# Optimization experiments

Hardware: AMD Instinct MI355X
Metric: run time of the kernel (lower is better)

## Reference

```python
import jax, jax.numpy as jnp
import numpy as np

N_NODES = 10000
N_EDGES = 160000
IN_DIM = 512
HID = 128
HEADS = 8
EMB = 256
NEG_SLOPE = 0.2  # PyG GATConv default


def setup_inputs() -> dict:
    key = jax.random.key(0)
    ks = jax.random.split(key, 12)
    x = jax.random.normal(ks[0], (N_NODES, IN_DIM), dtype=jnp.float32)
    edge_index = jax.random.randint(ks[1], (2, N_EDGES), 0, N_NODES, dtype=jnp.int64)
    s1 = 1.0 / np.sqrt(IN_DIM)
    s2 = 1.0 / np.sqrt(HEADS * HID)
    W1 = jax.random.normal(ks[2], (IN_DIM, HEADS * HID), dtype=jnp.float32) * s1
    a_src1 = jax.random.normal(ks[3], (HEADS, HID), dtype=jnp.float32) * s2
    a_dst1 = jax.random.normal(ks[4], (HEADS, HID), dtype=jnp.float32) * s2
    b1 = jnp.zeros((HEADS * HID,), dtype=jnp.float32)
    W2 = jax.random.normal(ks[5], (HEADS * HID, EMB), dtype=jnp.float32) * s2
    a_src2 = jax.random.normal(ks[6], (1, EMB), dtype=jnp.float32) * (1.0 / np.sqrt(EMB))
    a_dst2 = jax.random.normal(ks[7], (1, EMB), dtype=jnp.float32) * (1.0 / np.sqrt(EMB))
    b2 = jnp.zeros((EMB,), dtype=jnp.float32)
    return {"x": x, "edge_index": edge_index, "W1": W1, "a_src1": a_src1,
            "a_dst1": a_dst1, "b1": b1, "W2": W2, "a_src2": a_src2,
            "a_dst2": a_dst2, "b2": b2}


def gat_layer(h_in, src, dst, W, a_src, a_dst, b, concat, num_nodes):
    """PyG-style GATConv (eval mode, self-loops already in src/dst)."""
    H, C = a_src.shape
    h = (h_in @ W).reshape(num_nodes, H, C)            # [N, H, C]
    alpha_src = jnp.einsum('nhc,hc->nh', h, a_src)      # [N, H]
    alpha_dst = jnp.einsum('nhc,hc->nh', h, a_dst)      # [N, H]
    e = jax.nn.leaky_relu(alpha_src[src] + alpha_dst[dst], NEG_SLOPE)  # [E, H]
    # segment softmax over incoming edges of each destination node
    m = jax.ops.segment_max(e, dst, num_segments=num_nodes)            # [N, H]
    ex = jnp.exp(e - m[dst])
    denom = jax.ops.segment_sum(ex, dst, num_segments=num_nodes)       # [N, H]
    alpha = ex / denom[dst]                                            # [E, H]
    out = jax.ops.segment_sum(h[src] * alpha[:, :, None], dst,
                              num_segments=num_nodes)                  # [N, H, C]
    out = out.reshape(num_nodes, H * C) if concat else out.mean(axis=1)
    return out + b


def reference(x, edge_index, W1, a_src1, a_dst1, b1, W2, a_src2, a_dst2, b2):
    N = x.shape[0]
    loops = jnp.arange(N, dtype=edge_index.dtype)
    src = jnp.concatenate([edge_index[0], loops])
    dst = jnp.concatenate([edge_index[1], loops])
    h = gat_layer(x, src, dst, W1, a_src1, a_dst1, b1, concat=True, num_nodes=N)
    h = jax.nn.elu(h)  # dropout inactive in eval mode
    out = gat_layer(h, src, dst, W2, a_src2, a_dst2, b2, concat=False, num_nodes=N)
    return out
```

## Files before the change

kernel.cpp:

```cpp
#include <hip/hip_runtime.h>
#include <hip/hip_bf16.h>

typedef __attribute__((ext_vector_type(8))) short short8;
typedef __attribute__((ext_vector_type(4))) float floatx4;
typedef __attribute__((ext_vector_type(4))) unsigned short ushort4v;
typedef __attribute__((ext_vector_type(8))) unsigned short ushort8v;
typedef __attribute__((ext_vector_type(2))) unsigned int uint2v;
typedef __attribute__((ext_vector_type(4))) unsigned int uint4v;

#define NN 10000
#define E0 160000
#define ETOT (E0 + NN)
#define IN_DIM 512
#define HID1 1024
#define EMB 256
#define MPAD 10112
#define NX (NN * IN_DIM)
#define NW1 (IN_DIM * HID1)
#define NW2 (HID1 * EMB)
#define DETB 625

__device__ __forceinline__ float bf2f(unsigned short u) {
    unsigned v = ((unsigned)u) << 16;
    float f;
    __builtin_memcpy(&f, &v, 4);
    return f;
}
__device__ __forceinline__ float bflo(unsigned v) {
    unsigned x = v << 16;
    float f; __builtin_memcpy(&f, &x, 4);
    return f;
}
__device__ __forceinline__ float bfhi(unsigned v) {
    unsigned x = v & 0xffff0000u;
    float f; __builtin_memcpy(&f, &x, 4);
    return f;
}
__device__ __forceinline__ unsigned short f2bf(float f) {
    unsigned u;
    __builtin_memcpy(&u, &f, 4);
    unsigned lsb = (u >> 16) & 1;
    u += 0x7fff + lsb;
    return (unsigned short)(u >> 16);
}
__device__ __forceinline__ unsigned packbf(float lo, float hi) {
    return (unsigned)f2bf(lo) | ((unsigned)f2bf(hi) << 16);
}
__device__ __forceinline__ float loadf(const void* p, size_t i, int isf32) {
    if (isf32) return ((const float*)p)[i];
    return bf2f(((const unsigned short*)p)[i]);
}
__device__ __forceinline__ float lrelu(float e) { return e > 0.f ? e : 0.2f * e; }

__global__ void zero_kernel(int* p, int n) {
    int i = blockIdx.x * 256 + threadIdx.x;
    if (i < n) p[i] = 0;
}

__global__ __launch_bounds__(256) void probe_kernel(const int* ei32, const unsigned* xw,
                                                    int* eflag, int* isf32) {
    int t = threadIdx.x;
    if (blockIdx.x < DETB) {
        int i = blockIdx.x * 256 + t;
        int v = 0;
        int idx = 2 * i + 1;
        if (idx < 2 * E0) v = ei32[idx];
        unsigned long long any = __ballot(v != 0);
        if (any && (t & 63) == 0) atomicOr(eflag, 1);
    } else {
        __shared__ int cnt[256];
        int c = 0;
        #pragma unroll
        for (int j = 0; j < 16; ++j) {
            unsigned w = xw[t * 16 + j];
            int ex = (w >> 7) & 0xFF;
            if (ex >= 110 && ex <= 135) c++;
        }
        cnt[t] = c;
        __syncthreads();
        for (int off = 128; off > 0; off >>= 1) {
            if (t < off) cnt[t] += cnt[t + off];
            __syncthreads();
        }
        if (t == 0) *isf32 = (cnt[0] < 2048) ? 1 : 0;
    }
}

__device__ __forceinline__ int load_edge(const void* ei, long long idx, int m32) {
    if (m32) return ((const int*)ei)[idx];
    return (int)(((const long long*)ei)[idx]);
}

__global__ void count_kernel(const void* ei, const int* flag, int* counts) {
    int e = blockIdx.x * 256 + threadIdx.x;
    if (e < E0) {
        int m32 = (*flag != 0);
        int d = load_edge(ei, (long long)E0 + e, m32);
        if (d >= 0 && d < NN) atomicAdd(&counts[d], 1);
    }
}

__global__ __launch_bounds__(1024) void scan_kernel(const int* counts, int* offsets, int* cursor) {
    __shared__ int wsum[16];
    int t = threadIdx.x;
    int lane = t & 63, wv = t >> 6;
    int base = t * 10;
    int local[10];
    int s = 0;
    #pragma unroll
    for (int j = 0; j < 10; ++j) {
        int idx = base + j;
        int v = (idx < NN) ? (counts[idx] + 1) : 0;
        local[j] = v; s += v;
    }
    int v = s;
    #pragma unroll
    for (int d = 1; d < 64; d <<= 1) {
        int o = __shfl_up(v, d, 64);
        if (lane >= d) v += o;
    }
    if (lane == 63) wsum[wv] = v;
    __syncthreads();
    if (t < 16) {
        int w = wsum[t];
        #pragma unroll
        for (int d = 1; d < 16; d <<= 1) {
            int o = __shfl_up(w, d, 16);
            if (t >= d) w += o;
        }
        wsum[t] = w;
    }
    __syncthreads();
    int woff = (wv == 0) ? 0 : wsum[wv - 1];
    int run = woff + v - s;
    #pragma unroll
    for (int j = 0; j < 10; ++j) {
        int idx = base + j;
        if (idx < NN) { offsets[idx] = run; cursor[idx] = run; run += local[j]; }
    }
    if (t == 1023) offsets[NN] = wsum[15];
}

__global__ void scatter_kernel(const void* ei, const int* flag, int* cursor, int* csr_src) {
    int e = blockIdx.x * 256 + threadIdx.x;
    if (e >= ETOT) return;
    int m32 = (*flag != 0);
    int s, d;
    if (e < E0) { s = load_edge(ei, e, m32); d = load_edge(ei, (long long)E0 + e, m32); }
    else { s = d = e - E0; }
    if (s < 0) s = 0; if (s >= NN) s = NN - 1;
    if (d < 0) d = 0; if (d >= NN) d = NN - 1;
    int pos = atomicAdd(&cursor[d], 1);
    if (pos >= 0 && pos < ETOT) csr_src[pos] = s;
}

__global__ void convall_kernel(const void* x, const void* W1, const void* W2,
                               unsigned short* xb, unsigned short* W1t, unsigned short* W2t,
                               const int* isf32)
{
    int i = blockIdx.x * 256 + threadIdx.x;
    int f = *isf32;
    if (i < NX) { xb[i] = f2bf(loadf(x, i, f)); return; }
    i -= NX;
    if (i < NW1) {
        int r = i / HID1, c = i % HID1;
        W1t[(size_t)c * IN_DIM + r] = f2bf(loadf(W1, i, f));
        return;
    }
    i -= NW1;
    if (i < NW2) {
        int r = i / EMB, c = i % EMB;
        W2t[(size_t)c * HID1 + r] = f2bf(loadf(W2, i, f));
    }
}

template<bool OUTBF16>
__global__ __launch_bounds__(256) void gemm_tile(
    const unsigned short* __restrict__ A,
    const unsigned short* __restrict__ Bt,
    void* __restrict__ Cv,
    int N, int K)
{
    __shared__ unsigned short As[128 * 32];
    __shared__ unsigned short Bs[128 * 32];
    int t = threadIdx.x;
    int wave = t >> 6;
    int lane = t & 63;
    int quad = lane >> 4;
    int l16  = lane & 15;
    int mq = wave & 1, nq = wave >> 1;
    size_t mblk = (size_t)blockIdx.x * 128;
    size_t nblk = (size_t)blockIdx.y * 128;

    floatx4 acc[4][4];
    #pragma unroll
    for (int i = 0; i < 4; ++i)
        #pragma unroll
        for (int j = 0; j < 4; ++j)
            acc[i][j] = (floatx4){0.f, 0.f, 0.f, 0.f};

    const unsigned short* Abase = A + mblk * K;
    const unsigned short* Bbase = Bt + nblk * K;

    for (int kk = 0; kk < K; kk += 32) {
        __syncthreads();
        #pragma unroll
        for (int j = 0; j < 2; ++j) {
            int chunk = (wave << 7) + (j << 6) + lane;
            int r  = chunk >> 2;
            int cs = (chunk & 3) ^ (r & 3);
            const unsigned short* ga = Abase + (size_t)r * K + kk + cs * 8;
            const unsigned short* gb = Bbase + (size_t)r * K + kk + cs * 8;
            __builtin_amdgcn_global_load_lds(
                (const __attribute__((address_space(1))) void*)ga,
                (__attribute__((address_space(3))) void*)(As + (size_t)((wave << 7) + (j << 6)) * 8),
                16, 0, 0);
            __builtin_amdgcn_global_load_lds(
                (const __attribute__((address_space(1))) void*)gb,
                (__attribute__((address_space(3))) void*)(Bs + (size_t)((wave << 7) + (j << 6)) * 8),
                16, 0, 0);
        }
        __syncthreads();

        short8 af[4], bf[4];
        #pragma unroll
        for (int i = 0; i < 4; ++i) {
            int ar = mq * 64 + i * 16 + l16;
            int br = nq * 64 + i * 16 + l16;
            af[i] = *(const short8*)(const void*)(As + ar * 32 + (quad ^ (ar & 3)) * 8);
            bf[i] = *(const short8*)(const void*)(Bs + br * 32 + (quad ^ (br & 3)) * 8);
        }
        #pragma unroll
        for (int i = 0; i < 4; ++i)
            #pragma unroll
            for (int j = 0; j < 4; ++j)
                acc[i][j] = __builtin_amdgcn_mfma_f32_16x16x32_bf16(af[i], bf[j], acc[i][j], 0, 0, 0);
    }

    size_t crow0 = mblk + mq * 64 + quad * 4;
    size_t ccol0 = nblk + nq * 64 + l16;
    #pragma unroll
    for (int i = 0; i < 4; ++i) {
        #pragma unroll
        for (int r = 0; r < 4; ++r) {
            size_t row = crow0 + i * 16 + r;
            size_t b = row * N + ccol0;
            #pragma unroll
            for (int j = 0; j < 4; ++j) {
                if (OUTBF16) ((unsigned short*)Cv)[b + j * 16] = f2bf(acc[i][j][r]);
                else         ((float*)Cv)[b + j * 16] = acc[i][j][r];
            }
        }
    }
}

__global__ __launch_bounds__(256) void alpha1_kernel(
    const unsigned short* __restrict__ h1,
    const void* __restrict__ a_src, const void* __restrict__ a_dst,
    const int* __restrict__ isf32,
    float* __restrict__ as1, float* __restrict__ ad1)
{
    int n = blockIdx.x, t = threadIdx.x;
    int f = *isf32;
    ushort4v hv = *(const ushort4v*)(const void*)(h1 + (size_t)n * HID1 + t * 4);
    float ps = 0.f, pd = 0.f;
    #pragma unroll
    for (int i = 0; i < 4; ++i) {
        float h = bf2f(hv[i]);
        ps += h * loadf(a_src, t * 4 + i, f);
        pd += h * loadf(a_dst, t * 4 + i, f);
    }
    #pragma unroll
    for (int off = 1; off < 32; off <<= 1) {
        ps += __shfl_xor(ps, off, 64);
        pd += __shfl_xor(pd, off, 64);
    }
    if ((t & 31) == 0) {
        int h = t >> 5;
        as1[n * 8 + h] = ps;
        ad1[n * 8 + h] = pd;
    }
}

__global__ __launch_bounds__(256) void agg1_kernel(
    const unsigned short* __restrict__ h1, const int* __restrict__ offsets,
    const int* __restrict__ csr_src, const float* __restrict__ as1,
    const float* __restrict__ ad1, const void* __restrict__ b1,
    const int* __restrict__ isf32,
    unsigned short* __restrict__ hmid)
{
    int head = blockIdx.x & 7;
    int ng   = blockIdx.x >> 3;
    int n    = ng * 4 + (threadIdx.x >> 6);
    if (n >= NN) return;
    int lane = threadIdx.x & 63;
    int q    = lane >> 4;
    int sl   = lane & 15;
    int f = *isf32;
    int beg = offsets[n], end = offsets[n + 1];
    if (beg < 0) beg = 0; if (end > ETOT) end = ETOT;
    float ad = ad1[n * 8 + head];
    const unsigned* rb = (const unsigned*)h1 + head * 64 + sl * 4;
    const float* asb = as1 + head;

    float den = 0.f;
    float acc[8];
    #pragma unroll
    for (int j = 0; j < 8; ++j) acc[j] = 0.f;

    int i = beg + q;
    for (; i + 12 < end; i += 16) {
        int s0 = csr_src[i];      s0 &= 0x7fffffff; if (s0 >= NN) s0 = 0;
        int s1 = csr_src[i + 4];  s1 &= 0x7fffffff; if (s1 >= NN) s1 = 0;
        int s2 = csr_src[i + 8];  s2 &= 0x7fffffff; if (s2 >= NN) s2 = 0;
        int s3 = csr_src[i + 12]; s3 &= 0x7fffffff; if (s3 >= NN) s3 = 0;
        uint4v v0 = *(const uint4v*)(const void*)(rb + (size_t)s0 * 512);
        uint4v v1 = *(const uint4v*)(const void*)(rb + (size_t)s1 * 512);
        uint4v v2 = *(const uint4v*)(const void*)(rb + (size_t)s2 * 512);
        uint4v v3 = *(const uint4v*)(const void*)(rb + (size_t)s3 * 512);
        float w0 = __expf(lrelu(asb[s0 * 8] + ad));
        float w1 = __expf(lrelu(asb[s1 * 8] + ad));
        float w2 = __expf(lrelu(asb[s2 * 8] + ad));
        float w3 = __expf(lrelu(asb[s3 * 8] + ad));
        den += (w0 + w1) + (w2 + w3);
        #pragma unroll
        for (int k = 0; k < 4; ++k) {
            acc[2 * k]     += (bflo(v0[k]) * w0 + bflo(v1[k]) * w1) + (bflo(v2[k]) * w2 + bflo(v3[k]) * w3);
            acc[2 * k + 1] += (bfhi(v0[k]) * w0 + bfhi(v1[k]) * w1) + (bfhi(v2[k]) * w2 + bfhi(v3[k]) * w3);
        }
    }
    for (; i + 4 < end; i += 8) {
        int s0 = csr_src[i];     s0 &= 0x7fffffff; if (s0 >= NN) s0 = 0;
        int s1 = csr_src[i + 4]; s1 &= 0x7fffffff; if (s1 >= NN) s1 = 0;
        uint4v v0 = *(const uint4v*)(const void*)(rb + (size_t)s0 * 512);
        uint4v v1 = *(const uint4v*)(const void*)(rb + (size_t)s1 * 512);
        float w0 = __expf(lrelu(asb[s0 * 8] + ad));
        float w1 = __expf(lrelu(asb[s1 * 8] + ad));
        den += w0 + w1;
        #pragma unroll
        for (int k = 0; k < 4; ++k) {
            acc[2 * k]     += bflo(v0[k]) * w0 + bflo(v1[k]) * w1;
            acc[2 * k + 1] += bfhi(v0[k]) * w0 + bfhi(v1[k]) * w1;
        }
    }
    if (i < end) {
        int s0 = csr_src[i]; s0 &= 0x7fffffff; if (s0 >= NN) s0 = 0;
        uint4v v0 = *(const uint4v*)(const void*)(rb + (size_t)s0 * 512);
        float w0 = __expf(lrelu(asb[s0 * 8] + ad));
        den += w0;
        #pragma unroll
        for (int k = 0; k < 4; ++k) {
            acc[2 * k]     += bflo(v0[k]) * w0;
            acc[2 * k + 1] += bfhi(v0[k]) * w0;
        }
    }

    #pragma unroll
    for (int j = 0; j < 8; ++j) {
        acc[j] += __shfl_xor(acc[j], 16, 64);
        acc[j] += __shfl_xor(acc[j], 32, 64);
    }
    den += __shfl_xor(den, 16, 64);
    den += __shfl_xor(den, 32, 64);

    if (q == 0) {
        float rden = 1.0f / fmaxf(den, 1e-30f);
        int c0 = head * 128 + sl * 8;
        uint4v o;
        #pragma unroll
        for (int k = 0; k < 4; ++k) {
            float v0 = acc[2 * k]     * rden + loadf(b1, c0 + 2 * k, f);
            float v1 = acc[2 * k + 1] * rden + loadf(b1, c0 + 2 * k + 1, f);
            v0 = v0 > 0.f ? v0 : (__expf(v0) - 1.0f);
            v1 = v1 > 0.f ? v1 : (__expf(v1) - 1.0f);
            o[k] = packbf(v0, v1);
        }
        *(uint4v*)(void*)((unsigned*)hmid + (size_t)n * 512 + head * 64 + sl * 4) = o;
    }
}

__global__ __launch_bounds__(256) void alpha2_kernel(
    const unsigned short* __restrict__ h2,
    const void* __restrict__ a_src2, const void* __restrict__ a_dst2,
    const int* __restrict__ isf32,
    float* __restrict__ as2, float* __restrict__ ad2)
{
    int n = blockIdx.x, t = threadIdx.x;
    int f = *isf32;
    float v = bf2f(h2[(size_t)n * EMB + t]);
    float ps = v * loadf(a_src2, t, f);
    float pd = v * loadf(a_dst2, t, f);
    __shared__ float rs[256], rdm[256];
    rs[t] = ps; rdm[t] = pd;
    __syncthreads();
    for (int off = 128; off > 0; off >>= 1) {
        if (t < off) { rs[t] += rs[t + off]; rdm[t] += rdm[t + off]; }
        __syncthreads();
    }
    if (t == 0) { as2[n] = rs[0]; ad2[n] = rdm[0]; }
}

__global__ __launch_bounds__(256) void agg2_kernel(
    const unsigned short* __restrict__ h2, const int* __restrict__ offsets,
    const int* __restrict__ csr_src, const float* __restrict__ as2,
    const float* __restrict__ ad2, const void* __restrict__ b2,
    const int* __restrict__ isf32,
    float* __restrict__ out)
{
    int chunk = blockIdx.x & 3;
    int ng    = blockIdx.x >> 2;
    int n     = ng * 4 + (threadIdx.x >> 6);
    if (n >= NN) return;
    int lane = threadIdx.x & 63;
    int q    = lane >> 4;
    int sl   = lane & 15;
    int f = *isf32;
    int beg = offsets[n], end = offsets[n + 1];
    if (beg < 0) beg = 0; if (end > ETOT) end = ETOT;
    float adn = ad2[n];
    const unsigned* rb = (const unsigned*)h2 + chunk * 32 + sl * 2;

    float den = 0.f;
    float acc[4];
    #pragma unroll
    for (int j = 0; j < 4; ++j) acc[j] = 0.f;

    int i = beg + q;
    for (; i + 12 < end; i += 16) {
        int s0 = csr_src[i];      s0 &= 0x7fffffff; if (s0 >= NN) s0 = 0;
        int s1 = csr_src[i + 4];  s1 &= 0x7fffffff; if (s1 >= NN) s1 = 0;
        int s2 = csr_src[i + 8];  s2 &= 0x7fffffff; if (s2 >= NN) s2 = 0;
        int s3 = csr_src[i + 12]; s3 &= 0x7fffffff; if (s3 >= NN) s3 = 0;
        uint2v v0 = *(const uint2v*)(const void*)(rb + (size_t)s0 * 128);
        uint2v v1 = *(const uint2v*)(const void*)(rb + (size_t)s1 * 128);
        uint2v v2 = *(const uint2v*)(const void*)(rb + (size_t)s2 * 128);
        uint2v v3 = *(const uint2v*)(const void*)(rb + (size_t)s3 * 128);
        float w0 = __expf(lrelu(as2[s0] + adn));
        float w1 = __expf(lrelu(as2[s1] + adn));
        float w2 = __expf(lrelu(as2[s2] + adn));
        float w3 = __expf(lrelu(as2[s3] + adn));
        den += (w0 + w1) + (w2 + w3);
        acc[0] += (bflo(v0[0]) * w0 + bflo(v1[0]) * w1) + (bflo(v2[0]) * w2 + bflo(v3[0]) * w3);
        acc[1] += (bfhi(v0[0]) * w0 + bfhi(v1[0]) * w1) + (bfhi(v2[0]) * w2 + bfhi(v3[0]) * w3);
        acc[2] += (bflo(v0[1]) * w0 + bflo(v1[1]) * w1) + (bflo(v2[1]) * w2 + bflo(v3[1]) * w3);
        acc[3] += (bfhi(v0[1]) * w0 + bfhi(v1[1]) * w1) + (bfhi(v2[1]) * w2 + bfhi(v3[1]) * w3);
    }
    for (; i + 4 < end; i += 8) {
        int s0 = csr_src[i];     s0 &= 0x7fffffff; if (s0 >= NN) s0 = 0;
        int s1 = csr_src[i + 4]; s1 &= 0x7fffffff; if (s1 >= NN) s1 = 0;
        uint2v v0 = *(const uint2v*)(const void*)(rb + (size_t)s0 * 128);
        uint2v v1 = *(const uint2v*)(const void*)(rb + (size_t)s1 * 128);
        float w0 = __expf(lrelu(as2[s0] + adn));
        float w1 = __expf(lrelu(as2[s1] + adn));
        den += w0 + w1;
        acc[0] += bflo(v0[0]) * w0 + bflo(v1[0]) * w1;
        acc[1] += bfhi(v0[0]) * w0 + bfhi(v1[0]) * w1;
        acc[2] += bflo(v0[1]) * w0 + bflo(v1[1]) * w1;
        acc[3] += bfhi(v0[1]) * w0 + bfhi(v1[1]) * w1;
    }
    if (i < end) {
        int s0 = csr_src[i]; s0 &= 0x7fffffff; if (s0 >= NN) s0 = 0;
        uint2v v0 = *(const uint2v*)(const void*)(rb + (size_t)s0 * 128);
        float w0 = __expf(lrelu(as2[s0] + adn));
        den += w0;
        acc[0] += bflo(v0[0]) * w0;
        acc[1] += bfhi(v0[0]) * w0;
        acc[2] += bflo(v0[1]) * w0;
        acc[3] += bfhi(v0[1]) * w0;
    }

    #pragma unroll
    for (int j = 0; j < 4; ++j) {
        acc[j] += __shfl_xor(acc[j], 16, 64);
        acc[j] += __shfl_xor(acc[j], 32, 64);
    }
    den += __shfl_xor(den, 16, 64);
    den += __shfl_xor(den, 32, 64);

    if (q == 0) {
        float rden = 1.0f / fmaxf(den, 1e-30f);
        int c0 = chunk * 64 + sl * 4;
        floatx4 o;
        #pragma unroll
        for (int j = 0; j < 4; ++j)
            o[j] = acc[j] * rden + loadf(b2, c0 + j, f);
        *(floatx4*)(void*)(out + (size_t)n * EMB + c0) = o;
    }
}

extern "C" void kernel_launch(void* const* d_in, const int* in_sizes, int n_in,
                              void* d_out, int out_size, void* d_ws, size_t ws_size,
                              hipStream_t stream)
{
    const void* x      = d_in[0];
    const void* edge   = d_in[1];
    const void* W1     = d_in[2];
    const void* a_src1 = d_in[3];
    const void* a_dst1 = d_in[4];
    const void* b1     = d_in[5];
    const void* W2     = d_in[6];
    const void* a_src2 = d_in[7];
    const void* a_dst2 = d_in[8];
    const void* b2     = d_in[9];
    float* out = (float*)d_out;

    char* ws = (char*)d_ws;
    size_t off = 0;
    auto alloc = [&](size_t bytes) -> void* {
        void* p = ws + off;
        off += (bytes + 255) & ~(size_t)255;
        return p;
    };
    int*            counts = (int*)alloc((NN + 2) * 4);
    int*            offs   = (int*)alloc((NN + 1) * 4);
    int*            cursor = (int*)alloc(NN * 4);
    int*            csr    = (int*)alloc((size_t)ETOT * 4);
    float*          as1    = (float*)alloc((size_t)NN * 8 * 4);
    float*          ad1    = (float*)alloc((size_t)NN * 8 * 4);
    float*          as2    = (float*)alloc((size_t)NN * 4);
    float*          ad2    = (float*)alloc((size_t)NN * 4);
    unsigned short* xb     = (unsigned short*)alloc((size_t)MPAD * IN_DIM * 2);
    unsigned short* W1t    = (unsigned short*)alloc((size_t)IN_DIM * HID1 * 2);
    unsigned short* W2t    = (unsigned short*)alloc((size_t)HID1 * EMB * 2);
    unsigned short* h1b    = (unsigned short*)alloc((size_t)MPAD * HID1 * 2);
    unsigned short* hmid   = (unsigned short*)alloc((size_t)MPAD * HID1 * 2);
    unsigned short* h2b    = (unsigned short*)alloc((size_t)MPAD * EMB * 2);
    int* eflag = counts + NN;
    int* isf32 = counts + NN + 1;

    zero_kernel<<<(NN + 2 + 255) / 256, 256, 0, stream>>>(counts, NN + 2);
    probe_kernel<<<DETB + 1, 256, 0, stream>>>((const int*)edge, (const unsigned*)x, eflag, isf32);

    count_kernel<<<(E0 + 255) / 256, 256, 0, stream>>>(edge, eflag, counts);
    scan_kernel<<<1, 1024, 0, stream>>>(counts, offs, cursor);
    scatter_kernel<<<(ETOT + 255) / 256, 256, 0, stream>>>(edge, eflag, cursor, csr);

    convall_kernel<<<(NX + NW1 + NW2 + 255) / 256, 256, 0, stream>>>(
        x, W1, W2, xb, W1t, W2t, isf32);

    dim3 g1(MPAD / 128, HID1 / 128);
    gemm_tile<true><<<g1, 256, 0, stream>>>(xb, W1t, h1b, HID1, IN_DIM);

    alpha1_kernel<<<NN, 256, 0, stream>>>(h1b, a_src1, a_dst1, isf32, as1, ad1);
    agg1_kernel<<<(NN / 4) * 8, 256, 0, stream>>>(h1b, offs, csr, as1, ad1, b1, isf32, hmid);

    dim3 g2(MPAD / 128, EMB / 128);
    gemm_tile<true><<<g2, 256, 0, stream>>>(hmid, W2t, h2b, EMB, HID1);

    alpha2_kernel<<<NN, 256, 0, stream>>>(h2b, a_src2, a_dst2, isf32, as2, ad2);
    agg2_kernel<<<(NN / 4) * 4, 256, 0, stream>>>(h2b, offs, csr, as2, ad2, b2, isf32, out);
}
```

Measured before the change: 303.9 us.

## Precompute edge softmax weights and denominators in separate per-edge kernels

Adds ew1/ew2 kernels that compute the exp(leaky_relu) edge weights once per edge and head, writing them in CSR order and accumulating softmax denominators with atomics. The aggregation kernels then read these precomputed weights instead of recomputing exp and gathering alpha_src per edge. The lane mapping is also reshaped so each lane handles more channels (wider 32-byte loads) and 8 edge slots per wavefront. This costs two extra launches, extra memory traffic for the weight arrays and a csr_dst array, plus atomic contention on the denominators.

```diff
diff --git a/kernel.cpp b/kernel.cpp
--- a/kernel.cpp
+++ b/kernel.cpp
@@ -4,7 +4,6 @@
 typedef __attribute__((ext_vector_type(8))) short short8;
 typedef __attribute__((ext_vector_type(4))) float floatx4;
 typedef __attribute__((ext_vector_type(4))) unsigned short ushort4v;
-typedef __attribute__((ext_vector_type(8))) unsigned short ushort8v;
 typedef __attribute__((ext_vector_type(2))) unsigned int uint2v;
 typedef __attribute__((ext_vector_type(4))) unsigned int uint4v;
 
@@ -19,6 +18,7 @@
 #define NW1 (IN_DIM * HID1)
 #define NW2 (HID1 * EMB)
 #define DETB 625
+#define EPAD 170240
 
 __device__ __forceinline__ float bf2f(unsigned short u) {
     unsigned v = ((unsigned)u) << 16;
@@ -141,7 +141,8 @@
     if (t == 1023) offsets[NN] = wsum[15];
 }
 
-__global__ void scatter_kernel(const void* ei, const int* flag, int* cursor, int* csr_src) {
+__global__ void scatter_kernel(const void* ei, const int* flag, int* cursor,
+                               int* csr_src, int* csr_dst) {
     int e = blockIdx.x * 256 + threadIdx.x;
     if (e >= ETOT) return;
     int m32 = (*flag != 0);
@@ -151,7 +152,7 @@
     if (s < 0) s = 0; if (s >= NN) s = NN - 1;
     if (d < 0) d = 0; if (d >= NN) d = NN - 1;
     int pos = atomicAdd(&cursor[d], 1);
-    if (pos >= 0 && pos < ETOT) csr_src[pos] = s;
+    if (pos >= 0 && pos < ETOT) { csr_src[pos] = s; csr_dst[pos] = d; }
 }
 
 __global__ void convall_kernel(const void* x, const void* W1, const void* W2,
@@ -282,10 +283,25 @@
     }
 }
 
+__global__ __launch_bounds__(256) void ew1_kernel(
+    const int* __restrict__ csr_src, const int* __restrict__ csr_dst,
+    const float* __restrict__ as1, const float* __restrict__ ad1,
+    float* __restrict__ ew1, float* __restrict__ den1)
+{
+    int e = blockIdx.x * 256 + threadIdx.x;
+    if (e >= ETOT) return;
+    int h = blockIdx.y;
+    int s = csr_src[e]; s &= 0x7fffffff; if (s >= NN) s = 0;
+    int d = csr_dst[e]; d &= 0x7fffffff; if (d >= NN) d = 0;
+    float w = __expf(lrelu(as1[s * 8 + h] + ad1[d * 8 + h]));
+    ew1[(size_t)h * EPAD + e] = w;
+    atomicAdd(&den1[d * 8 + h], w);
+}
+
 __global__ __launch_bounds__(256) void agg1_kernel(
     const unsigned short* __restrict__ h1, const int* __restrict__ offsets,
-    const int* __restrict__ csr_src, const float* __restrict__ as1,
-    const float* __restrict__ ad1, const void* __restrict__ b1,
+    const int* __restrict__ csr_src, const float* __restrict__ ew1,
+    const float* __restrict__ den1, const void* __restrict__ b1,
     const int* __restrict__ isf32,
     unsigned short* __restrict__ hmid)
 {
@@ -294,88 +310,98 @@
     int n    = ng * 4 + (threadIdx.x >> 6);
     if (n >= NN) return;
     int lane = threadIdx.x & 63;
-    int q    = lane >> 4;
-    int sl   = lane & 15;
+    int oc   = lane >> 3;
+    int sl   = lane & 7;
     int f = *isf32;
     int beg = offsets[n], end = offsets[n + 1];
     if (beg < 0) beg = 0; if (end > ETOT) end = ETOT;
-    float ad = ad1[n * 8 + head];
-    const unsigned* rb = (const unsigned*)h1 + head * 64 + sl * 4;
-    const float* asb = as1 + head;
-
-    float den = 0.f;
-    float acc[8];
-    #pragma unroll
-    for (int j = 0; j < 8; ++j) acc[j] = 0.f;
-
-    int i = beg + q;
-    for (; i + 12 < end; i += 16) {
+    const unsigned* rb = (const unsigned*)h1 + head * 64 + sl * 8;
+    const float* ewh = ew1 + (size_t)head * EPAD;
+
+    float acc[16];
+    #pragma unroll
+    for (int j = 0; j < 16; ++j) acc[j] = 0.f;
+
+    int i = beg + oc;
+    for (; i + 24 < end; i += 32) {
         int s0 = csr_src[i];      s0 &= 0x7fffffff; if (s0 >= NN) s0 = 0;
-        int s1 = csr_src[i + 4];  s1 &= 0x7fffffff; if (s1 >= NN) s1 = 0;
-        int s2 = csr_src[i + 8];  s2 &= 0x7fffffff; if (s2 >= NN) s2 = 0;
-        int s3 = csr_src[i + 12]; s3 &= 0x7fffffff; if (s3 >= NN) s3 = 0;
-        uint4v v0 = *(const uint4v*)(const void*)(rb + (size_t)s0 * 512);
-        uint4v v1 = *(const uint4v*)(const void*)(rb + (size_t)s1 * 512);
-        uint4v v2 = *(const uint4v*)(const void*)(rb + (size_t)s2 * 512);
-        uint4v v3 = *(const uint4v*)(const void*)(rb + (size_t)s3 * 512);
-        float w0 = __expf(lrelu(asb[s0 * 8] + ad));
-        float w1 = __expf(lrelu(asb[s1 * 8] + ad));
-        float w2 = __expf(lrelu(asb[s2 * 8] + ad));
-        float w3 = __expf(lrelu(asb[s3 * 8] + ad));
-        den += (w0 + w1) + (w2 + w3);
-        #pragma unroll
-        for (int k = 0; k < 4; ++k) {
-            acc[2 * k]     += (bflo(v0[k]) * w0 + bflo(v1[k]) * w1) + (bflo(v2[k]) * w2 + bflo(v3[k]) * w3);
-            acc[2 * k + 1] += (bfhi(v0[k]) * w0 + bfhi(v1[k]) * w1) + (bfhi(v2[k]) * w2 + bfhi(v3[k]) * w3);
-        }
-    }
-    for (; i + 4 < end; i += 8) {
+        int s1 = csr_src[i + 8];  s1 &= 0x7fffffff; if (s1 >= NN) s1 = 0;
+        int s2 = csr_src[i + 16]; s2 &= 0x7fffffff; if (s2 >= NN) s2 = 0;
+        int s3 = csr_src[i + 24]; s3 &= 0x7fffffff; if (s3 >= NN) s3 = 0;
+        uint4v a0 = *(const uint4v*)(const void*)(rb + (size_t)s0 * 512);
+        uint4v c0v = *(const uint4v*)(const void*)(rb + (size_t)s0 * 512 + 4);
+        uint4v a1 = *(const uint4v*)(const void*)(rb + (size_t)s1 * 512);
+        uint4v c1v = *(const uint4v*)(const void*)(rb + (size_t)s1 * 512 + 4);
+        uint4v a2 = *(const uint4v*)(const void*)(rb + (size_t)s2 * 512);
+        uint4v c2v = *(const uint4v*)(const void*)(rb + (size_t)s2 * 512 + 4);
+        uint4v a3 = *(const uint4v*)(const void*)(rb + (size_t)s3 * 512);
+        uint4v c3v = *(const uint4v*)(const void*)(rb + (size_t)s3 * 512 + 4);
+        float w0 = ewh[i], w1 = ewh[i + 8], w2 = ewh[i + 16], w3 = ewh[i + 24];
+        #pragma unroll
+        for (int k = 0; k < 4; ++k) {
+            acc[2 * k]      += (bflo(a0[k]) * w0 + bflo(a1[k]) * w1) + (bflo(a2[k]) * w2 + bflo(a3[k]) * w3);
+            acc[2 * k + 1]  += (bfhi(a0[k]) * w0 + bfhi(a1[k]) * w1) + (bfhi(a2[k]) * w2 + bfhi(a3[k]) * w3);
+            acc[8 + 2 * k]  += (bflo(c0v[k]) * w0 + bflo(c1v[k]) * w1) + (bflo(c2v[k]) * w2 + bflo(c3v[k]) * w3);
+            acc[9 + 2 * k]  += (bfhi(c0v[k]) * w0 + bfhi(c1v[k]) * w1) + (bfhi(c2v[k]) * w2 + bfhi(c3v[k]) * w3);
+        }
+    }
+    for (; i + 8 < end; i += 16) {
         int s0 = csr_src[i];     s0 &= 0x7fffffff; if (s0 >= NN) s0 = 0;
-        int s1 = csr_src[i + 4]; s1 &= 0x7fffffff; if (s1 >= NN) s1 = 0;
-        uint4v v0 = *(const uint4v*)(const void*)(rb + (size_t)s0 * 512);
-        uint4v v1 = *(const uint4v*)(const void*)(rb + (size_t)s1 * 512);
-        float w0 = __expf(lrelu(asb[s0 * 8] + ad));
-        float w1 = __expf(lrelu(asb[s1 * 8] + ad));
-        den += w0 + w1;
-        #pragma unroll
-        for (int k = 0; k < 4; ++k) {
-            acc[2 * k]     += bflo(v0[k]) * w0 + bflo(v1[k]) * w1;
-            acc[2 * k + 1] += bfhi(v0[k]) * w0 + bfhi(v1[k]) * w1;
+        int s1 = csr_src[i + 8]; s1 &= 0x7fffffff; if (s1 >= NN) s1 = 0;
+        uint4v a0 = *(const uint4v*)(const void*)(rb + (size_t)s0 * 512);
+        uint4v c0v = *(const uint4v*)(const void*)(rb + (size_t)s0 * 512 + 4);
+        uint4v a1 = *(const uint4v*)(const void*)(rb + (size_t)s1 * 512);
+        uint4v c1v = *(const uint4v*)(const void*)(rb + (size_t)s1 * 512 + 4);
+        float w0 = ewh[i], w1 = ewh[i + 8];
+        #pragma unroll
+        for (int k = 0; k < 4; ++k) {
+            acc[2 * k]      += bflo(a0[k]) * w0 + bflo(a1[k]) * w1;
+            acc[2 * k + 1]  += bfhi(a0[k]) * w0 + bfhi(a1[k]) * w1;
+            acc[8 + 2 * k]  += bflo(c0v[k]) * w0 + bflo(c1v[k]) * w1;
+            acc[9 + 2 * k]  += bfhi(c0v[k]) * w0 + bfhi(c1v[k]) * w1;
         }
     }
     if (i < end) {
         int s0 = csr_src[i]; s0 &= 0x7fffffff; if (s0 >= NN) s0 = 0;
-        uint4v v0 = *(const uint4v*)(const void*)(rb + (size_t)s0 * 512);
-        float w0 = __expf(lrelu(asb[s0 * 8] + ad));
-        den += w0;
-        #pragma unroll
-        for (int k = 0; k < 4; ++k) {
-            acc[2 * k]     += bflo(v0[k]) * w0;
-            acc[2 * k + 1] += bfhi(v0[k]) * w0;
-        }
-    }
-
-    #pragma unroll
-    for (int j = 0; j < 8; ++j) {
+        uint4v a0 = *(const uint4v*)(const void*)(rb + (size_t)s0 * 512);
+        uint4v c0v = *(const uint4v*)(const void*)(rb + (size_t)s0 * 512 + 4);
+        float w0 = ewh[i];
+        #pragma unroll
+        for (int k = 0; k < 4; ++k) {
+            acc[2 * k]      += bflo(a0[k]) * w0;
+            acc[2 * k + 1]  += bfhi(a0[k]) * w0;
+            acc[8 + 2 * k]  += bflo(c0v[k]) * w0;
+            acc[9 + 2 * k]  += bfhi(c0v[k]) * w0;
+        }
+    }
+
+    #pragma unroll
+    for (int j = 0; j < 16; ++j) {
+        acc[j] += __shfl_xor(acc[j], 8, 64);
         acc[j] += __shfl_xor(acc[j], 16, 64);
         acc[j] += __shfl_xor(acc[j], 32, 64);
     }
-    den += __shfl_xor(den, 16, 64);
-    den += __shfl_xor(den, 32, 64);
-
-    if (q == 0) {
-        float rden = 1.0f / fmaxf(den, 1e-30f);
-        int c0 = head * 128 + sl * 8;
-        uint4v o;
+
+    if (oc == 0) {
+        float rden = 1.0f / fmaxf(den1[n * 8 + head], 1e-30f);
+        int c0 = head * 128 + sl * 16;
+        uint4v oA, oB;
         #pragma unroll
         for (int k = 0; k < 4; ++k) {
             float v0 = acc[2 * k]     * rden + loadf(b1, c0 + 2 * k, f);
             float v1 = acc[2 * k + 1] * rden + loadf(b1, c0 + 2 * k + 1, f);
             v0 = v0 > 0.f ? v0 : (__expf(v0) - 1.0f);
             v1 = v1 > 0.f ? v1 : (__expf(v1) - 1.0f);
-            o[k] = packbf(v0, v1);
-        }
-        *(uint4v*)(void*)((unsigned*)hmid + (size_t)n * 512 + head * 64 + sl * 4) = o;
+            oA[k] = packbf(v0, v1);
+            float u0 = acc[8 + 2 * k] * rden + loadf(b1, c0 + 8 + 2 * k, f);
+            float u1 = acc[9 + 2 * k] * rden + loadf(b1, c0 + 9 + 2 * k, f);
+            u0 = u0 > 0.f ? u0 : (__expf(u0) - 1.0f);
+            u1 = u1 > 0.f ? u1 : (__expf(u1) - 1.0f);
+            oB[k] = packbf(u0, u1);
+        }
+        unsigned* hw = (unsigned*)hmid;
+        *(uint4v*)(void*)(hw + (size_t)n * 512 + head * 64 + sl * 8)     = oA;
+        *(uint4v*)(void*)(hw + (size_t)n * 512 + head * 64 + sl * 8 + 4) = oB;
     }
 }
 
@@ -400,10 +426,24 @@
     if (t == 0) { as2[n] = rs[0]; ad2[n] = rdm[0]; }
 }
 
+__global__ __launch_bounds__(256) void ew2_kernel(
+    const int* __restrict__ csr_src, const int* __restrict__ csr_dst,
+    const float* __restrict__ as2, const float* __restrict__ ad2,
+    float* __restrict__ ew2, float* __restrict__ den2)
+{
+    int e = blockIdx.x * 256 + threadIdx.x;
+    if (e >= ETOT) return;
+    int s = csr_src[e]; s &= 0x7fffffff; if (s >= NN) s = 0;
+    int d = csr_dst[e]; d &= 0x7fffffff; if (d >= NN) d = 0;
+    float w = __expf(lrelu(as2[s] + ad2[d]));
+    ew2[e] = w;
+    atomicAdd(&den2[d], w);
+}
+
 __global__ __launch_bounds__(256) void agg2_kernel(
     const unsigned short* __restrict__ h2, const int* __restrict__ offsets,
-    const int* __restrict__ csr_src, const float* __restrict__ as2,
-    const float* __restrict__ ad2, const void* __restrict__ b2,
+    const int* __restrict__ csr_src, const float* __restrict__ ew2,
+    const float* __restrict__ den2, const void* __restrict__ b2,
     const int* __restrict__ isf32,
     float* __restrict__ out)
 {
@@ -412,79 +452,75 @@
     int n     = ng * 4 + (threadIdx.x >> 6);
     if (n >= NN) return;
     int lane = threadIdx.x & 63;
-    int q    = lane >> 4;
-    int sl   = lane & 15;
+    int oc   = lane >> 3;
+    int sl   = lane & 7;
     int f = *isf32;
     int beg = offsets[n], end = offsets[n + 1];
     if (beg < 0) beg = 0; if (end > ETOT) end = ETOT;
-    float adn = ad2[n];
-    const unsigned* rb = (const unsigned*)h2 + chunk * 32 + sl * 2;
-
-    float den = 0.f;
-    float acc[4];
-    #pragma unroll
-    for (int j = 0; j < 4; ++j) acc[j] = 0.f;
-
-    int i = beg + q;
-    for (; i + 12 < end; i += 16) {
+    const unsigned* rb = (const unsigned*)h2 + chunk * 32 + sl * 4;
+
+    float acc[8];
+    #pragma unroll
+    for (int j = 0; j < 8; ++j) acc[j] = 0.f;
+
+    int i = beg + oc;
+    for (; i + 24 < end; i += 32) {
         int s0 = csr_src[i];      s0 &= 0x7fffffff; if (s0 >= NN) s0 = 0;
-        int s1 = csr_src[i + 4];  s1 &= 0x7fffffff; if (s1 >= NN) s1 = 0;
-        int s2 = csr_src[i + 8];  s2 &= 0x7fffffff; if (s2 >= NN) s2 = 0;
-        int s3 = csr_src[i + 12]; s3 &= 0x7fffffff; if (s3 >= NN) s3 = 0;
-        uint2v v0 = *(const uint2v*)(const void*)(rb + (size_t)s0 * 128);
-        uint2v v1 = *(const uint2v*)(const void*)(rb + (size_t)s1 * 128);
-        uint2v v2 = *(const uint2v*)(const void*)(rb + (size_t)s2 * 128);
-        uint2v v3 = *(const uint2v*)(const void*)(rb + (size_t)s3 * 128);
-        float w0 = __expf(lrelu(as2[s0] + adn));
-        float w1 = __expf(lrelu(as2[s1] + adn));
-        float w2 = __expf(lrelu(as2[s2] + adn));
-        float w3 = __expf(lrelu(as2[s3] + adn));
-        den += (w0 + w1) + (w2 + w3);
-        acc[0] += (bflo(v0[0]) * w0 + bflo(v1[0]) * w1) + (bflo(v2[0]) * w2 + bflo(v3[0]) * w3);
-        acc[1] += (bfhi(v0[0]) * w0 + bfhi(v1[0]) * w1) + (bfhi(v2[0]) * w2 + bfhi(v3[0]) * w3);
-        acc[2] += (bflo(v0[1]) * w0 + bflo(v1[1]) * w1) + (bflo(v2[1]) * w2 + bflo(v3[1]) * w3);
-        acc[3] += (bfhi(v0[1]) * w0 + bfhi(v1[1]) * w1) + (bfhi(v2[1]) * w2 + bfhi(v3[1]) * w3);
-    }
-    for (; i + 4 < end; i += 8) {
+        int s1 = csr_src[i + 8];  s1 &= 0x7fffffff; if (s1 >= NN) s1 = 0;
+        int s2 = csr_src[i + 16]; s2 &= 0x7fffffff; if (s2 >= NN) s2 = 0;
+        int s3 = csr_src[i + 24]; s3 &= 0x7fffffff; if (s3 >= NN) s3 = 0;
+        uint4v v0 = *(const uint4v*)(const void*)(rb + (size_t)s0 * 128);
+        uint4v v1 = *(const uint4v*)(const void*)(rb + (size_t)s1 * 128);
+        uint4v v2 = *(const uint4v*)(const void*)(rb + (size_t)s2 * 128);
+        uint4v v3 = *(const uint4v*)(const void*)(rb + (size_t)s3 * 128);
+        float w0 = ew2[i], w1 = ew2[i + 8], w2 = ew2[i + 16], w3 = ew2[i + 24];
+        #pragma unroll
+        for (int k = 0; k < 4; ++k) {
+            acc[2 * k]     += (bflo(v0[k]) * w0 + bflo(v1[k]) * w1) + (bflo(v2[k]) * w2 + bflo(v3[k]) * w3);
+            acc[2 * k + 1] += (bfhi(v0[k]) * w0 + bfhi(v1[k]) * w1) + (bfhi(v2[k]) * w2 + bfhi(v3[k]) * w3);
+        }
+    }
+    for (; i + 8 < end; i += 16) {
         int s0 = csr_src[i];     s0 &= 0x7fffffff; if (s0 >= NN) s0 = 0;
-        int s1 = csr_src[i + 4]; s1 &= 0x7fffffff; if (s1 >= NN) s1 = 0;
-        uint2v v0 = *(const uint2v*)(const void*)(rb + (size_t)s0 * 128);
-        uint2v v1 = *(const uint2v*)(const void*)(rb + (size_t)s1 * 128);
-        float w0 = __expf(lrelu(as2[s0] + adn));
-        float w1 = __expf(lrelu(as2[s1] + adn));
-        den += w0 + w1;
-        acc[0] += bflo(v0[0]) * w0 + bflo(v1[0]) * w1;
-        acc[1] += bfhi(v0[0]) * w0 + bfhi(v1[0]) * w1;
-        acc[2] += bflo(v0[1]) * w0 + bflo(v1[1]) * w1;
-        acc[3] += bfhi(v0[1]) * w0 + bfhi(v1[1]) * w1;
+        int s1 = csr_src[i + 8]; s1 &= 0x7fffffff; if (s1 >= NN) s1 = 0;
+        uint4v v0 = *(const uint4v*)(const void*)(rb + (size_t)s0 * 128);
+        uint4v v1 = *(const uint4v*)(const void*)(rb + (size_t)s1 * 128);
+        float w0 = ew2[i], w1 = ew2[i + 8];
+        #pragma unroll
+        for (int k = 0; k < 4; ++k) {
+            acc[2 * k]     += bflo(v0[k]) * w0 + bflo(v1[k]) * w1;
+            acc[2 * k + 1] += bfhi(v0[k]) * w0 + bfhi(v1[k]) * w1;
+        }
     }
     if (i < end) {
         int s0 = csr_src[i]; s0 &= 0x7fffffff; if (s0 >= NN) s0 = 0;
-        uint2v v0 = *(const uint2v*)(const void*)(rb + (size_t)s0 * 128);
-        float w0 = __expf(lrelu(as2[s0] + adn));
-        den += w0;
-        acc[0] += bflo(v0[0]) * w0;
-        acc[1] += bfhi(v0[0]) * w0;
-        acc[2] += bflo(v0[1]) * w0;
-        acc[3] += bfhi(v0[1]) * w0;
-    }
-
-    #pragma unroll
-    for (int j = 0; j < 4; ++j) {
+        uint4v v0 = *(const uint4v*)(const void*)(rb + (size_t)s0 * 128);
+        float w0 = ew2[i];
+        #pragma unroll
+        for (int k = 0; k < 4; ++k) {
+            acc[2 * k]     += bflo(v0[k]) * w0;
+            acc[2 * k + 1] += bfhi(v0[k]) * w0;
+        }
+    }
+
+    #pragma unroll
+    for (int j = 0; j < 8; ++j) {
+        acc[j] += __shfl_xor(acc[j], 8, 64);
         acc[j] += __shfl_xor(acc[j], 16, 64);
         acc[j] += __shfl_xor(acc[j], 32, 64);
     }
-    den += __shfl_xor(den, 16, 64);
-    den += __shfl_xor(den, 32, 64);
-
-    if (q == 0) {
-        float rden = 1.0f / fmaxf(den, 1e-30f);
-        int c0 = chunk * 64 + sl * 4;
-        floatx4 o;
-        #pragma unroll
-        for (int j = 0; j < 4; ++j)
-            o[j] = acc[j] * rden + loadf(b2, c0 + j, f);
-        *(floatx4*)(void*)(out + (size_t)n * EMB + c0) = o;
+
+    if (oc == 0) {
+        float rden = 1.0f / fmaxf(den2[n], 1e-30f);
+        int c0 = chunk * 64 + sl * 8;
+        floatx4 o0, o1;
+        #pragma unroll
+        for (int j = 0; j < 4; ++j) {
+            o0[j] = acc[j]     * rden + loadf(b2, c0 + j, f);
+            o1[j] = acc[4 + j] * rden + loadf(b2, c0 + 4 + j, f);
+        }
+        *(floatx4*)(void*)(out + (size_t)n * EMB + c0)     = o0;
+        *(floatx4*)(void*)(out + (size_t)n * EMB + c0 + 4) = o1;
     }
 }
 
@@ -512,13 +548,19 @@
         return p;
     };
     int*            counts = (int*)alloc((NN + 2) * 4);
+    float*          den1   = (float*)alloc((size_t)NN * 8 * 4);
+    float*          den2   = (float*)alloc((size_t)NN * 4);
+    int             zspan  = (int)(((char*)den2 - (char*)counts) / 4) + NN;
     int*            offs   = (int*)alloc((NN + 1) * 4);
     int*            cursor = (int*)alloc(NN * 4);
     int*            csr    = (int*)alloc((size_t)ETOT * 4);
+    int*            csrd   = (int*)alloc((size_t)ETOT * 4);
     float*          as1    = (float*)alloc((size_t)NN * 8 * 4);
     float*          ad1    = (float*)alloc((size_t)NN * 8 * 4);
     float*          as2    = (float*)alloc((size_t)NN * 4);
     float*          ad2    = (float*)alloc((size_t)NN * 4);
+    float*          ew1    = (float*)alloc((size_t)8 * EPAD * 4);
+    float*          ew2    = (float*)alloc((size_t)EPAD * 4);
     unsigned short* xb     = (unsigned short*)alloc((size_t)MPAD * IN_DIM * 2);
     unsigned short* W1t    = (unsigned short*)alloc((size_t)IN_DIM * HID1 * 2);
     unsigned short* W2t    = (unsigned short*)alloc((size_t)HID1 * EMB * 2);
@@ -528,12 +570,12 @@
     int* eflag = counts + NN;
     int* isf32 = counts + NN + 1;
 
-    zero_kernel<<<(NN + 2 + 255) / 256, 256, 0, stream>>>(counts, NN + 2);
+    zero_kernel<<<(zspan + 255) / 256, 256, 0, stream>>>(counts, zspan);
     probe_kernel<<<DETB + 1, 256, 0, stream>>>((const int*)edge, (const unsigned*)x, eflag, isf32);
 
     count_kernel<<<(E0 + 255) / 256, 256, 0, stream>>>(edge, eflag, counts);
     scan_kernel<<<1, 1024, 0, stream>>>(counts, offs, cursor);
-    scatter_kernel<<<(ETOT + 255) / 256, 256, 0, stream>>>(edge, eflag, cursor, csr);
+    scatter_kernel<<<(ETOT + 255) / 256, 256, 0, stream>>>(edge, eflag, cursor, csr, csrd);
 
     convall_kernel<<<(NX + NW1 + NW2 + 255) / 256, 256, 0, stream>>>(
         x, W1, W2, xb, W1t, W2t, isf32);
@@ -542,11 +584,14 @@
     gemm_tile<true><<<g1, 256, 0, stream>>>(xb, W1t, h1b, HID1, IN_DIM);
 
     alpha1_kernel<<<NN, 256, 0, stream>>>(h1b, a_src1, a_dst1, isf32, as1, ad1);
-    agg1_kernel<<<(NN / 4) * 8, 256, 0, stream>>>(h1b, offs, csr, as1, ad1, b1, isf32, hmid);
+    dim3 ge1((ETOT + 255) / 256, 8);
+    ew1_kernel<<<ge1, 256, 0, stream>>>(csr, csrd, as1, ad1, ew1, den1);
+    agg1_kernel<<<(NN / 4) * 8, 256, 0, stream>>>(h1b, offs, csr, ew1, den1, b1, isf32, hmid);
 
     dim3 g2(MPAD / 128, EMB / 128);
     gemm_tile<true><<<g2, 256, 0, stream>>>(hmid, W2t, h2b, EMB, HID1);
 
     alpha2_kernel<<<NN, 256, 0, stream>>>(h2b, a_src2, a_dst2, isf32, as2, ad2);
-    agg2_kernel<<<(NN / 4) * 4, 256, 0, stream>>>(h2b, offs, csr, as2, ad2, b2, isf32, out);
-}
+    ew2_kernel<<<(ETOT + 255) / 256, 256, 0, stream>>>(csr, csrd, as2, ad2, ew2, den2);
+    agg2_kernel<<<(NN / 4) * 4, 256, 0, stream>>>(h2b, offs, csr, ew2, den2, b2, isf32, out);
+}
```

New measurement: 430.3 us. 41.6% more time.
